# Performance work log

Measured on AMD Instinct MI355X. Metric: run time of the kernel, lower is better.

Reference implementation:

```python
import jax, jax.numpy as jnp
import numpy as np

B, T, C, H, W = 2, 8, 256, 24, 24
NH = 8
HC = C // NH          # 32 head channels
KT, KHW = 3, 9        # offset conv kernel
ST, SHW = 2, 8        # offset conv stride
EPS = 1e-5


def _p(key, shape):
    return jax.random.normal(key, shape, dtype=jnp.float32) * 0.05


def setup_inputs() -> dict:
    ks = jax.random.split(jax.random.key(0), 16)
    return {
        "x": jax.random.normal(ks[0], (B, T, C, H, W), dtype=jnp.float32),
        "w_in": _p(ks[1], (C, C)), "b_in": _p(ks[2], (C,)),
        "w_q": _p(ks[3], (C, C)), "b_q": _p(ks[4], (C,)),
        "w_off_dw": _p(ks[5], (HC, 1, KT, KHW, KHW)), "b_off_dw": _p(ks[6], (HC,)),
        "ln_g": jnp.ones((HC,), jnp.float32), "ln_b": jnp.zeros((HC,), jnp.float32),
        "w_off_proj": _p(ks[7], (3, HC)),
        "w_k": _p(ks[8], (C, C)), "b_k": _p(ks[9], (C,)),
        "w_v": _p(ks[10], (C, C)), "b_v": _p(ks[11], (C,)),
        "rpe_w1": _p(ks[12], (32, 3)), "rpe_b1": _p(ks[13], (32,)),
        "rpe_w2": _p(ks[14], (1, 32)),
    }


def _conv1x1(x, w, b):
    # x: (B,C,T,H,W), w: (Co,Ci) -> pointwise Conv3d
    return jnp.einsum('bcthw,oc->bothw', x, w) + b[None, :, None, None, None]


def _trilinear(img, gx, gy, gz):
    # torch F.grid_sample(mode='bilinear', align_corners=True) for 5D input.
    # img: (G,Ch,T,H,W); gx->W axis, gy->H axis, gz->T axis, coords in [-1,1], shape (G,S)
    G, Ch, Td, Hd, Wd = img.shape
    ix = (gx + 1.0) * 0.5 * (Wd - 1)
    iy = (gy + 1.0) * 0.5 * (Hd - 1)
    iz = (gz + 1.0) * 0.5 * (Td - 1)
    x0 = jnp.floor(ix); y0 = jnp.floor(iy); z0 = jnp.floor(iz)
    fx = ix - x0; fy = iy - y0; fz = iz - z0
    x0i = jnp.clip(x0.astype(jnp.int32), 0, Wd - 1); x1i = jnp.clip(x0i + 1, 0, Wd - 1)
    y0i = jnp.clip(y0.astype(jnp.int32), 0, Hd - 1); y1i = jnp.clip(y0i + 1, 0, Hd - 1)
    z0i = jnp.clip(z0.astype(jnp.int32), 0, Td - 1); z1i = jnp.clip(z0i + 1, 0, Td - 1)
    bidx = jnp.arange(G)[:, None]

    def g(zi, yi, xi):
        return img[bidx, :, zi, yi, xi]  # (G,S,Ch)

    wz0, wz1 = (1.0 - fz)[..., None], fz[..., None]
    wy0, wy1 = (1.0 - fy)[..., None], fy[..., None]
    wx0, wx1 = (1.0 - fx)[..., None], fx[..., None]
    return (g(z0i, y0i, x0i) * wz0 * wy0 * wx0 + g(z0i, y0i, x1i) * wz0 * wy0 * wx1 +
            g(z0i, y1i, x0i) * wz0 * wy1 * wx0 + g(z0i, y1i, x1i) * wz0 * wy1 * wx1 +
            g(z1i, y0i, x0i) * wz1 * wy0 * wx0 + g(z1i, y0i, x1i) * wz1 * wy0 * wx1 +
            g(z1i, y1i, x0i) * wz1 * wy1 * wx0 + g(z1i, y1i, x1i) * wz1 * wy1 * wx1)


def reference(x, w_in, b_in, w_q, b_q, w_off_dw, b_off_dw, ln_g, ln_b, w_off_proj,
              w_k, b_k, w_v, b_v, rpe_w1, rpe_b1, rpe_w2):
    scale = HC ** (-0.5)
    xc = _conv1x1(jnp.transpose(x, (0, 2, 1, 3, 4)), w_in, b_in)       # (B,C,T,H,W)
    q = _conv1x1(xc, w_q, b_q)
    q_off = q.reshape(B * NH, HC, T, H, W)
    # depthwise offset conv: kernel (3,9,9), stride (2,8,8), pad (1,4,4)
    off = jax.lax.conv_general_dilated(
        q_off, w_off_dw, (ST, SHW, SHW),
        ((KT // 2, KT // 2), (KHW // 2, KHW // 2), (KHW // 2, KHW // 2)),
        dimension_numbers=('NCDHW', 'OIDHW', 'NCDHW'), feature_group_count=HC)
    off = off + b_off_dw[None, :, None, None, None]
    Tk, Hk, Wk = off.shape[2], off.shape[3], off.shape[4]
    o = jnp.transpose(off, (0, 2, 3, 4, 1))                             # (G,Tk,Hk,Wk,HC)
    mu = o.mean(-1, keepdims=True)
    var = ((o - mu) ** 2).mean(-1, keepdims=True)
    o = (o - mu) / jnp.sqrt(var + EPS) * ln_g + ln_b
    o = jax.nn.gelu(o, approximate=False)
    offset = jnp.einsum('bthwc,pc->bthwp', o, w_off_proj)               # (G,Tk,Hk,Wk,3)
    # reference points (linspace(0.5, K-0.5, K) normalized by (K-1))
    rt = ((jnp.arange(Tk, dtype=jnp.float32) + 0.5) / (Tk - 1.0)) * 2.0 - 1.0
    ry = ((jnp.arange(Hk, dtype=jnp.float32) + 0.5) / (Hk - 1.0)) * 2.0 - 1.0
    rx = ((jnp.arange(Wk, dtype=jnp.float32) + 0.5) / (Wk - 1.0)) * 2.0 - 1.0
    ref = jnp.stack(jnp.meshgrid(rt, ry, rx, indexing='ij'), axis=-1)   # (Tk,Hk,Wk,3)
    pos = jnp.clip(offset + ref, -1.0, 1.0)                             # offset_range_factor < 0 path
    G = B * NH
    n = Tk * Hk * Wk
    m = T * H * W
    posf = pos.reshape(G, n, 3)                                         # (t, y, x)
    # torch passes grid = pos[..., (0,2,1)] -> grid (x_w, y_h, z_t) = (pos_t, pos_x, pos_y)
    xs = _trilinear(xc.reshape(G, HC, T, H, W), posf[..., 0], posf[..., 2], posf[..., 1])  # (G,n,HC)
    x_sampled = jnp.transpose(xs, (0, 2, 1)).reshape(B, C, Tk, Hk, Wk)
    k = _conv1x1(x_sampled, w_k, b_k).reshape(G, HC, n)
    v = _conv1x1(x_sampled, w_v, b_v).reshape(G, HC, n)
    qf = q.reshape(G, HC, m)
    attn = jnp.einsum('bcm,bcn->bmn', qf, k) * scale                    # (G,m,n)
    # log-CPB bias (source normalizes y by W-1 and x by H-1; faithful)
    qt = (jnp.arange(T, dtype=jnp.float32) / (T - 1.0)) * 2.0 - 1.0
    qy = (jnp.arange(H, dtype=jnp.float32) / (W - 1.0)) * 2.0 - 1.0
    qx = (jnp.arange(W, dtype=jnp.float32) / (H - 1.0)) * 2.0 - 1.0
    qg = jnp.stack(jnp.meshgrid(qt, qy, qx, indexing='ij'), axis=-1).reshape(m, 3)
    disp = (qg[None, :, None, :] - posf[:, None, :, :]) * 4.0           # (G,m,n,3)
    disp = jnp.sign(disp) * jnp.log2(jnp.abs(disp) + 1.0) / 3.0         # log2(8) = 3
    hbias = jax.nn.relu(jnp.einsum('gmnp,hp->gmnh', disp, rpe_w1) + rpe_b1)
    attn = attn + jnp.einsum('gmnh,oh->gmno', hbias, rpe_w2)[..., 0]
    attn = jax.nn.softmax(attn, axis=2)
    out = jnp.einsum('bmn,bcn->bcm', attn, v).reshape(B, C, T, H, W)
    return jnp.transpose(out, (0, 2, 1, 3, 4))                          # (B,T,C,H,W)
```

## Files before the change

kernel.cpp:

```cpp
#include <hip/hip_runtime.h>
#include <hip/hip_bf16.h>

typedef unsigned short ushortT;
typedef __attribute__((ext_vector_type(8))) short bf16x8;
typedef __attribute__((ext_vector_type(4))) float f32x4;
typedef __fp16 half2v __attribute__((ext_vector_type(2)));

#define WS_XC   0
#define WS_QB   2359296
#define WS_POS  3538944
#define WS_K    3540736
#define WS_V    3559168
#define WS_WC   3577600
#define WS_B512 3675904
#define WS_BIAS 3676416

__device__ __forceinline__ float bf2f(ushortT u) {
  union { unsigned int i; float f; } c; c.i = ((unsigned int)u) << 16; return c.f;
}
__device__ __forceinline__ ushortT f2bf(float f) {
  union { float f; unsigned int i; } c; c.f = f;
  unsigned int lsb = (c.i >> 16) & 1;
  return (ushortT)((c.i + 0x7fff + lsb) >> 16);
}
__device__ __forceinline__ float ldg_f(const void* p, int i, int bf) {
  return bf ? bf2f(((const ushortT*)p)[i]) : ((const float*)p)[i];
}
__device__ __forceinline__ int detect_bf(const void* x) {
  const ushortT* u = (const ushortT*)x;
  int wild = 0;
#pragma unroll
  for (int i = 0; i < 32; i++) {
    int e = (u[i] >> 7) & 0xFF;
    wild += (e != 0 && (e < 90 || e > 160)) ? 1 : 0;
  }
  return wild <= 4;
}
__device__ __forceinline__ float logmap(float d) {
  return copysignf(__log2f(fabsf(d) + 1.f) * (1.f / 3.f), d);
}

__global__ __launch_bounds__(256) void k_wc(const void* x, const void* w_in, const void* b_in,
                                            const void* w_q, const void* b_q,
                                            float* wc, float* bias512) {
  int o = blockIdx.x, tid = threadIdx.x;
  int bf = detect_bf(x);
  __shared__ float wq_s[256];
  __shared__ float red[256];
  wq_s[tid] = ldg_f(w_q, o * 256 + tid, bf);
  __syncthreads();
  float s = 0.f;
#pragma unroll 8
  for (int j = 0; j < 256; j++) s += wq_s[j] * ldg_f(w_in, j * 256 + tid, bf);
  wc[o * 256 + tid] = s;
  red[tid] = wq_s[tid] * ldg_f(b_in, tid, bf);
  __syncthreads();
  for (int m = 128; m; m >>= 1) {
    if (tid < m) red[tid] += red[tid + m];
    __syncthreads();
  }
  if (tid == 0) bias512[256 + o] = red[0] + ldg_f(b_q, o, bf);
  if (o == 0) bias512[tid] = ldg_f(b_in, tid, bf);
}

__global__ __launch_bounds__(256) void k_gemm_mfma(const void* x, const void* w_in, const float* wc,
                                                   const float* bias512, float* xc, ushortT* qb) {
  const int bf = detect_bf(x);
  __shared__ ushortT Ah[2][64 * 40], Al[2][64 * 40];
  __shared__ ushortT Bh[2][64 * 40], Bl[2][64 * 40];
  int tid = threadIdx.x;
  int bid = blockIdx.x;
  int colT = bid / 144, rowT = bid % 144;
  int col0 = colT * 64;
  int row0 = rowT * 64;
  int bt = row0 / 576;
  int hw0 = row0 % 576;
  const int isW = (col0 < 256);
  const ushortT* xB = (const ushortT*)x;
  const float*   xF = (const float*)x;
  const ushortT* wB = (const ushortT*)w_in;
  const float*   wF = (const float*)w_in;
  int ar = tid & 63, aoct = tid >> 6;
  int bn = tid >> 2, bko = tid & 3;
  int w = tid >> 6, l = tid & 63;
  int wr = w >> 1, wcq = w & 1;
  int lr = l & 15, lk = l >> 4;
  f32x4 acc[2][2] = {};

  float va[8], vb[8];
  auto loadA = [&](int kt) {
    int kbase = (bt * 256 + kt * 32 + aoct * 8) * 576 + hw0 + ar;
#pragma unroll
    for (int j = 0; j < 8; j++)
      va[j] = bf ? bf2f(xB[kbase + j * 576]) : xF[kbase + j * 576];
  };
  auto loadB = [&](int kt) {
    if (isW) {
      if (bf) {
        const ushortT* pp = wB + (col0 + bn) * 256 + kt * 32 + bko * 8;
#pragma unroll
        for (int j = 0; j < 8; j++) vb[j] = bf2f(pp[j]);
      } else {
        const float* pp = wF + (col0 + bn) * 256 + kt * 32 + bko * 8;
        float4 f0 = *(const float4*)pp;
        float4 f1 = *(const float4*)(pp + 4);
        vb[0] = f0.x; vb[1] = f0.y; vb[2] = f0.z; vb[3] = f0.w;
        vb[4] = f1.x; vb[5] = f1.y; vb[6] = f1.z; vb[7] = f1.w;
      }
    } else {
      const float* pp = wc + (col0 - 256 + bn) * 256 + kt * 32 + bko * 8;
      float4 f0 = *(const float4*)pp;
      float4 f1 = *(const float4*)(pp + 4);
      vb[0] = f0.x; vb[1] = f0.y; vb[2] = f0.z; vb[3] = f0.w;
      vb[4] = f1.x; vb[5] = f1.y; vb[6] = f1.z; vb[7] = f1.w;
    }
  };
  auto writeAB = [&](int buf) {
    unsigned ua[8], ra[8];
#pragma unroll
    for (int j = 0; j < 8; j++) {
      ua[j] = __float_as_uint(va[j]);
      ra[j] = __float_as_uint(va[j] - __uint_as_float(ua[j] & 0xffff0000u));
    }
    int4 ph, pl;
    ph.x = (int)((ua[0] >> 16) | (ua[1] & 0xffff0000u));
    ph.y = (int)((ua[2] >> 16) | (ua[3] & 0xffff0000u));
    ph.z = (int)((ua[4] >> 16) | (ua[5] & 0xffff0000u));
    ph.w = (int)((ua[6] >> 16) | (ua[7] & 0xffff0000u));
    pl.x = (int)((ra[0] >> 16) | (ra[1] & 0xffff0000u));
    pl.y = (int)((ra[2] >> 16) | (ra[3] & 0xffff0000u));
    pl.z = (int)((ra[4] >> 16) | (ra[5] & 0xffff0000u));
    pl.w = (int)((ra[6] >> 16) | (ra[7] & 0xffff0000u));
    *(int4*)&Ah[buf][ar * 40 + aoct * 8] = ph;
    *(int4*)&Al[buf][ar * 40 + aoct * 8] = pl;
#pragma unroll
    for (int j = 0; j < 8; j++) {
      ua[j] = __float_as_uint(vb[j]);
      ra[j] = __float_as_uint(vb[j] - __uint_as_float(ua[j] & 0xffff0000u));
    }
    ph.x = (int)((ua[0] >> 16) | (ua[1] & 0xffff0000u));
    ph.y = (int)((ua[2] >> 16) | (ua[3] & 0xffff0000u));
    ph.z = (int)((ua[4] >> 16) | (ua[5] & 0xffff0000u));
    ph.w = (int)((ua[6] >> 16) | (ua[7] & 0xffff0000u));
    pl.x = (int)((ra[0] >> 16) | (ra[1] & 0xffff0000u));
    pl.y = (int)((ra[2] >> 16) | (ra[3] & 0xffff0000u));
    pl.z = (int)((ra[4] >> 16) | (ra[5] & 0xffff0000u));
    pl.w = (int)((ra[6] >> 16) | (ra[7] & 0xffff0000u));
    *(int4*)&Bh[buf][bn * 40 + bko * 8] = ph;
    *(int4*)&Bl[buf][bn * 40 + bko * 8] = pl;
  };

  loadA(0); loadB(0);
  writeAB(0);
  __syncthreads();
  for (int kt = 0; kt < 8; kt++) {
    int cur = kt & 1;
    if (kt < 7) { loadA(kt + 1); loadB(kt + 1); }
    bf16x8 a0h = *(const bf16x8*)&Ah[cur][(wr * 32 + 0 * 16 + lr) * 40 + lk * 8];
    bf16x8 a1h = *(const bf16x8*)&Ah[cur][(wr * 32 + 1 * 16 + lr) * 40 + lk * 8];
    bf16x8 a0l = *(const bf16x8*)&Al[cur][(wr * 32 + 0 * 16 + lr) * 40 + lk * 8];
    bf16x8 a1l = *(const bf16x8*)&Al[cur][(wr * 32 + 1 * 16 + lr) * 40 + lk * 8];
    bf16x8 b0h = *(const bf16x8*)&Bh[cur][(wcq * 32 + 0 * 16 + lr) * 40 + lk * 8];
    bf16x8 b1h = *(const bf16x8*)&Bh[cur][(wcq * 32 + 1 * 16 + lr) * 40 + lk * 8];
    bf16x8 b0l = *(const bf16x8*)&Bl[cur][(wcq * 32 + 0 * 16 + lr) * 40 + lk * 8];
    bf16x8 b1l = *(const bf16x8*)&Bl[cur][(wcq * 32 + 1 * 16 + lr) * 40 + lk * 8];
    acc[0][0] = __builtin_amdgcn_mfma_f32_16x16x32_bf16(a0h, b0h, acc[0][0], 0, 0, 0);
    acc[0][0] = __builtin_amdgcn_mfma_f32_16x16x32_bf16(a0h, b0l, acc[0][0], 0, 0, 0);
    acc[0][0] = __builtin_amdgcn_mfma_f32_16x16x32_bf16(a0l, b0h, acc[0][0], 0, 0, 0);
    acc[0][1] = __builtin_amdgcn_mfma_f32_16x16x32_bf16(a0h, b1h, acc[0][1], 0, 0, 0);
    acc[0][1] = __builtin_amdgcn_mfma_f32_16x16x32_bf16(a0h, b1l, acc[0][1], 0, 0, 0);
    acc[0][1] = __builtin_amdgcn_mfma_f32_16x16x32_bf16(a0l, b1h, acc[0][1], 0, 0, 0);
    acc[1][0] = __builtin_amdgcn_mfma_f32_16x16x32_bf16(a1h, b0h, acc[1][0], 0, 0, 0);
    acc[1][0] = __builtin_amdgcn_mfma_f32_16x16x32_bf16(a1h, b0l, acc[1][0], 0, 0, 0);
    acc[1][0] = __builtin_amdgcn_mfma_f32_16x16x32_bf16(a1l, b0h, acc[1][0], 0, 0, 0);
    acc[1][1] = __builtin_amdgcn_mfma_f32_16x16x32_bf16(a1h, b1h, acc[1][1], 0, 0, 0);
    acc[1][1] = __builtin_amdgcn_mfma_f32_16x16x32_bf16(a1h, b1l, acc[1][1], 0, 0, 0);
    acc[1][1] = __builtin_amdgcn_mfma_f32_16x16x32_bf16(a1l, b1h, acc[1][1], 0, 0, 0);
    if (kt < 7) writeAB(cur ^ 1);
    __syncthreads();
  }
#pragma unroll
  for (int m = 0; m < 2; m++) {
#pragma unroll
    for (int n = 0; n < 2; n++) {
#pragma unroll
      for (int i = 0; i < 4; i++) {
        int row = row0 + wr * 32 + m * 16 + lk * 4 + i;
        int col = col0 + wcq * 32 + n * 16 + lr;
        float v = acc[m][n][i] + bias512[col];
        if (isW) xc[row * 256 + col] = v;
        else     qb[row * 256 + (col - 256)] = f2bf(v);
      }
    }
  }
}

__global__ __launch_bounds__(256) void k_offsets(const void* x, const ushortT* qb, const void* w_dw,
                                                 const void* b_dw, const void* ln_g, const void* ln_b,
                                                 const void* w_proj, const void* rpe_w1,
                                                 const void* rpe_b1, const void* rpe_w2,
                                                 float* pos, float* biastab) {
  __shared__ float wdw[243 * 33];
  __shared__ float part[8][33];
  __shared__ float ptile[3];
  __shared__ float dts[56];
  int bid = blockIdx.x;
  int g = bid / 36, nn = bid % 36;
  int b = g >> 3, nh = g & 7;
  int tk = nn / 9, hk = (nn / 3) % 3, wk = nn % 3;
  int tid = threadIdx.x;
  int ch = tid & 31, grp = tid >> 5;
  int bf = detect_bf(x);
  for (int i = tid; i < 7776; i += 256) {
    int c = i / 243, tap = i % 243;
    wdw[tap * 33 + c] = ldg_f(w_dw, i, bf);
  }
  __syncthreads();
  float sum = 0.f;
  for (int tap = grp; tap < 243; tap += 8) {
    int dt = tap / 81, rem = tap % 81, dh = rem / 9, dw = rem % 9;
    int t = tk * 2 - 1 + dt, h = hk * 8 - 4 + dh, w = wk * 8 - 4 + dw;
    if (t < 0 || t >= 8 || h < 0 || h >= 24 || w < 0 || w >= 24) continue;
    float qv = bf2f(qb[((b * 8 + t) * 576 + h * 24 + w) * 256 + nh * 32 + ch]);
    sum += qv * wdw[tap * 33 + ch];
  }
  part[grp][ch] = sum;
  __syncthreads();
  if (tid < 32) {
    float v = ldg_f(b_dw, ch, bf);
#pragma unroll
    for (int j = 0; j < 8; j++) v += part[j][ch];
    float s1 = v;
    for (int m = 16; m; m >>= 1) s1 += __shfl_xor(s1, m);
    float mu = s1 * (1.f / 32.f);
    float d = v - mu;
    float s2 = d * d;
    for (int m = 16; m; m >>= 1) s2 += __shfl_xor(s2, m);
    float o = d * rsqrtf(s2 * (1.f / 32.f) + 1e-5f) * ldg_f(ln_g, ch, bf) + ldg_f(ln_b, ch, bf);
    o = 0.5f * o * (1.f + erff(o * 0.70710678118654752f));
    float res[3];
#pragma unroll
    for (int p = 0; p < 3; p++) {
      float t3 = o * ldg_f(w_proj, p * 32 + ch, bf);
      for (int m = 16; m; m >>= 1) t3 += __shfl_xor(t3, m);
      res[p] = t3;
    }
    if (ch == 0) {
      float ref0 = ((tk + 0.5f) / 3.f) * 2.f - 1.f;
      float ref1 = ((hk + 0.5f) / 2.f) * 2.f - 1.f;
      float ref2 = ((wk + 0.5f) / 2.f) * 2.f - 1.f;
      float p0 = fminf(1.f, fmaxf(-1.f, res[0] + ref0));
      float p1 = fminf(1.f, fmaxf(-1.f, res[1] + ref1));
      float p2 = fminf(1.f, fmaxf(-1.f, res[2] + ref2));
      pos[bid * 3 + 0] = p0;
      pos[bid * 3 + 1] = p1;
      pos[bid * 3 + 2] = p2;
      ptile[0] = p0; ptile[1] = p1; ptile[2] = p2;
    }
  }
  __syncthreads();
  if (tid < 56) {
    float dv;
    if (tid < 8)       dv = ((float)tid        * (2.f / 7.f)  - 1.f - ptile[0]) * 4.f;
    else if (tid < 32) dv = ((float)(tid - 8)  * (2.f / 23.f) - 1.f - ptile[1]) * 4.f;
    else               dv = ((float)(tid - 32) * (2.f / 23.f) - 1.f - ptile[2]) * 4.f;
    dts[tid] = logmap(dv);
  }
  __syncthreads();
  half2v wxp[16], wyp[16], wzp[16], wbp[16], w2p[16];
#pragma unroll
  for (int j = 0; j < 16; j++) {
    wxp[j] = __builtin_amdgcn_cvt_pkrtz(ldg_f(rpe_w1, (2*j)*3+0, bf), ldg_f(rpe_w1, (2*j+1)*3+0, bf));
    wyp[j] = __builtin_amdgcn_cvt_pkrtz(ldg_f(rpe_w1, (2*j)*3+1, bf), ldg_f(rpe_w1, (2*j+1)*3+1, bf));
    wzp[j] = __builtin_amdgcn_cvt_pkrtz(ldg_f(rpe_w1, (2*j)*3+2, bf), ldg_f(rpe_w1, (2*j+1)*3+2, bf));
    wbp[j] = __builtin_amdgcn_cvt_pkrtz(ldg_f(rpe_b1, 2*j, bf), ldg_f(rpe_b1, 2*j+1, bf));
    w2p[j] = __builtin_amdgcn_cvt_pkrtz(ldg_f(rpe_w2, 2*j, bf), ldg_f(rpe_w2, 2*j+1, bf));
  }
  half2v zero = __builtin_amdgcn_cvt_pkrtz(0.f, 0.f);
  float* brow = biastab + bid * 4608;
  for (int mm = tid; mm < 4608; mm += 256) {
    int t = mm / 576, hw = mm % 576, hh = hw / 24, ww = hw % 24;
    float d0 = dts[t], d1 = dts[8 + hh], d2 = dts[32 + ww];
    half2v d0h = __builtin_amdgcn_cvt_pkrtz(d0, d0);
    half2v d1h = __builtin_amdgcn_cvt_pkrtz(d1, d1);
    half2v d2h = __builtin_amdgcn_cvt_pkrtz(d2, d2);
    float s = 0.f;
#pragma unroll
    for (int j = 0; j < 16; j++) {
      half2v hb = d0h * wxp[j] + (d1h * wyp[j] + (d2h * wzp[j] + wbp[j]));
      half2v r;
      asm("v_pk_max_f16 %0, %1, %2" : "=v"(r) : "v"(hb), "v"(zero));
      asm("v_dot2_f32_f16 %0, %1, %2, %0" : "+v"(s) : "v"(r), "v"(w2p[j]));
    }
    brow[mm] = s;
  }
}

__global__ __launch_bounds__(256) void k_svkv(const void* x, const float* xc_rm, const float* pos,
                                              const void* w_k, const void* b_k,
                                              const void* w_v, const void* b_v,
                                              float* k_rm, float* v_rm) {
  int bx = blockIdx.x;
  int row = bx >> 2, quad = bx & 3;
  int sel = quad >> 1, colhalf = quad & 1;
  int b = row / 36, nn = row % 36;
  int tid = threadIdx.x;
  int bf = detect_bf(x);
  __shared__ float a[256];
  {
    int nh = tid >> 5;
    int g = b * 8 + nh;
    float p0 = pos[(g * 36 + nn) * 3 + 0];
    float p1 = pos[(g * 36 + nn) * 3 + 1];
    float p2 = pos[(g * 36 + nn) * 3 + 2];
    float ix = (p0 + 1.f) * 0.5f * 23.f;
    float iy = (p2 + 1.f) * 0.5f * 23.f;
    float iz = (p1 + 1.f) * 0.5f * 7.f;
    float x0f = floorf(ix), y0f = floorf(iy), z0f = floorf(iz);
    float fx = ix - x0f, fy = iy - y0f, fz = iz - z0f;
    int x0 = min(max((int)x0f, 0), 23), x1 = min(x0 + 1, 23);
    int y0 = min(max((int)y0f, 0), 23), y1 = min(y0 + 1, 23);
    int z0 = min(max((int)z0f, 0), 7),  z1 = min(z0 + 1, 7);
#define AT(z, y, x) xc_rm[(((b * 8 + (z)) * 576 + (y) * 24 + (x)) * 256 + tid)]
    a[tid] =
      AT(z0, y0, x0) * (1.f - fz) * (1.f - fy) * (1.f - fx) + AT(z0, y0, x1) * (1.f - fz) * (1.f - fy) * fx +
      AT(z0, y1, x0) * (1.f - fz) * fy * (1.f - fx)         + AT(z0, y1, x1) * (1.f - fz) * fy * fx +
      AT(z1, y0, x0) * fz * (1.f - fy) * (1.f - fx)         + AT(z1, y0, x1) * fz * (1.f - fy) * fx +
      AT(z1, y1, x0) * fz * fy * (1.f - fx)                 + AT(z1, y1, x1) * fz * fy * fx;
#undef AT
  }
  __syncthreads();
  const void* w = sel ? w_v : w_k;
  const void* bb = sel ? b_v : b_k;
  int col = colhalf * 128 + (tid >> 1);
  int half = tid & 1;
  int c0 = half * 128;
  float s = 0.f;
  if (bf) {
    const ushortT* wp = (const ushortT*)w + col * 256 + c0;
#pragma unroll 4
    for (int c = 0; c < 128; c += 8) {
      ushort4 k0 = *(const ushort4*)(wp + c), k1 = *(const ushort4*)(wp + c + 4);
      s += a[c0+c+0]*bf2f(k0.x) + a[c0+c+1]*bf2f(k0.y) + a[c0+c+2]*bf2f(k0.z) + a[c0+c+3]*bf2f(k0.w)
         + a[c0+c+4]*bf2f(k1.x) + a[c0+c+5]*bf2f(k1.y) + a[c0+c+6]*bf2f(k1.z) + a[c0+c+7]*bf2f(k1.w);
    }
  } else {
    const float* wp = (const float*)w + col * 256 + c0;
#pragma unroll 8
    for (int c = 0; c < 128; c += 4) {
      float4 k4 = *(const float4*)(wp + c);
      s += a[c0+c]*k4.x + a[c0+c+1]*k4.y + a[c0+c+2]*k4.z + a[c0+c+3]*k4.w;
    }
  }
  s += __shfl_xor(s, 1);
  if (half == 0) {
    float* outp = sel ? v_rm : k_rm;
    outp[row * 256 + col] = s + ldg_f(bb, col, bf);
  }
}

__global__ __launch_bounds__(256) void k_attn(const void* x, const ushortT* qb,
                                              const float* k_rm, const float* v_rm,
                                              const float* biastab, void* outp) {
  __shared__ ushortT ksb[36][32];
  __shared__ ushortT vsb[36][32];
  int g = blockIdx.y, b = g >> 3, nh = g & 7;
  int tid = threadIdx.x;
  int bf = detect_bf(x);
  for (int e = tid; e < 36 * 32; e += 256) {
    int nn = e >> 5, ch = e & 31;
    ksb[nn][ch] = f2bf(k_rm[(b * 36 + nn) * 256 + nh * 32 + ch]);
    vsb[nn][ch] = f2bf(v_rm[(b * 36 + nn) * 256 + nh * 32 + ch]);
  }
  __syncthreads();

  int sub = tid & 7, chb = sub * 4;
  int mm = blockIdx.x * 32 + (tid >> 3);
  int t = mm / 576, hw = mm % 576;
  float qreg[4];
  {
    ushort4 u = *(const ushort4*)&qb[(b * 4608 + mm) * 256 + nh * 32 + chb];
    qreg[0] = bf2f(u.x); qreg[1] = bf2f(u.y); qreg[2] = bf2f(u.z); qreg[3] = bf2f(u.w);
  }
  const float scale = 0.17677669529663687f;
  const float* brow = biastab + g * 36 * 4608 + mm;
  float p[36];
#pragma unroll
  for (int nn = 0; nn < 36; nn++) {
    ushort4 k4 = *(const ushort4*)&ksb[nn][chb];
    float s = qreg[0] * bf2f(k4.x) + qreg[1] * bf2f(k4.y)
            + qreg[2] * bf2f(k4.z) + qreg[3] * bf2f(k4.w);
    p[nn] = s * scale;
  }
#pragma unroll
  for (int nn = 0; nn < 36; nn++) {
    p[nn] += __shfl_xor(p[nn], 1);
    p[nn] += __shfl_xor(p[nn], 2);
    p[nn] += __shfl_xor(p[nn], 4);
    p[nn] += brow[nn * 4608];
  }
  float mx = -1e30f;
#pragma unroll
  for (int nn = 0; nn < 36; nn++) mx = fmaxf(mx, p[nn]);
  float se = 0.f;
#pragma unroll
  for (int nn = 0; nn < 36; nn++) {
    float e = __expf(p[nn] - mx);
    p[nn] = e;
    se += e;
  }
  float inv = 1.f / se;
  float acc[4] = {};
#pragma unroll
  for (int nn = 0; nn < 36; nn++) {
    float pr = p[nn] * inv;
    ushort4 v4 = *(const ushort4*)&vsb[nn][chb];
    acc[0] += pr * bf2f(v4.x); acc[1] += pr * bf2f(v4.y);
    acc[2] += pr * bf2f(v4.z); acc[3] += pr * bf2f(v4.w);
  }
  int obase = ((b * 8 + t) * 256 + nh * 32 + chb) * 576 + hw;
  if (bf) {
    __hip_bfloat16* o = (__hip_bfloat16*)outp;
#pragma unroll
    for (int j = 0; j < 4; j++) o[obase + j * 576] = __float2bfloat16(acc[j]);
  } else {
    float* o = (float*)outp;
#pragma unroll
    for (int j = 0; j < 4; j++) o[obase + j * 576] = acc[j];
  }
}

extern "C" void kernel_launch(void* const* d_in, const int* in_sizes, int n_in,
                              void* d_out, int out_size, void* d_ws, size_t ws_size,
                              hipStream_t stream) {
  const void* x        = d_in[0];
  const void* w_in     = d_in[1];
  const void* b_in     = d_in[2];
  const void* w_q      = d_in[3];
  const void* b_q      = d_in[4];
  const void* w_off_dw = d_in[5];
  const void* b_off_dw = d_in[6];
  const void* ln_g     = d_in[7];
  const void* ln_b     = d_in[8];
  const void* w_off_pj = d_in[9];
  const void* w_k      = d_in[10];
  const void* b_k      = d_in[11];
  const void* w_v      = d_in[12];
  const void* b_v      = d_in[13];
  const void* rpe_w1   = d_in[14];
  const void* rpe_b1   = d_in[15];
  const void* rpe_w2   = d_in[16];

  float* ws     = (float*)d_ws;
  float* xc     = ws + WS_XC;
  ushortT* qb   = (ushortT*)(ws + WS_QB);
  float* pos    = ws + WS_POS;
  float* krm    = ws + WS_K;
  float* vrm    = ws + WS_V;
  float* wcf    = ws + WS_WC;
  float* b512   = ws + WS_B512;
  float* biastab = ws + WS_BIAS;

  k_wc<<<256, 256, 0, stream>>>(x, w_in, b_in, w_q, b_q, wcf, b512);
  k_gemm_mfma<<<1152, 256, 0, stream>>>(x, w_in, wcf, b512, xc, qb);
  k_offsets<<<576, 256, 0, stream>>>(x, qb, w_off_dw, b_off_dw, ln_g, ln_b, w_off_pj,
                                     rpe_w1, rpe_b1, rpe_w2, pos, biastab);
  k_svkv<<<288, 256, 0, stream>>>(x, xc, pos, w_k, b_k, w_v, b_v, krm, vrm);
  k_attn<<<dim3(144, 16), 256, 0, stream>>>(x, qb, krm, vrm, biastab, d_out);
}
```

Before: 124.1 us.

## Split RPE bias table computation into separate high-parallelism kernel

The log-CPB bias table generation moves out of k_offsets into a new k_biastab kernel launched over 8x576 blocks, one per time slice per offset tile. k_offsets now only writes the 56 log-mapped displacement values per tile to a workspace table. The new kernel also hoists the time-axis term (d0*w_x + b1) out of the inner loop. This spreads the bias work across many more blocks, at the cost of an extra kernel launch and a small intermediate buffer.

```diff
diff --git a/kernel.cpp b/kernel.cpp
--- a/kernel.cpp
+++ b/kernel.cpp
@@ -13,7 +13,8 @@
 #define WS_V    3559168
 #define WS_WC   3577600
 #define WS_B512 3675904
-#define WS_BIAS 3676416
+#define WS_DTAB 3676416
+#define WS_BIAS 3709184
 
 __device__ __forceinline__ float bf2f(ushortT u) {
   union { unsigned int i; float f; } c; c.i = ((unsigned int)u) << 16; return c.f;
@@ -197,13 +198,10 @@
 
 __global__ __launch_bounds__(256) void k_offsets(const void* x, const ushortT* qb, const void* w_dw,
                                                  const void* b_dw, const void* ln_g, const void* ln_b,
-                                                 const void* w_proj, const void* rpe_w1,
-                                                 const void* rpe_b1, const void* rpe_w2,
-                                                 float* pos, float* biastab) {
+                                                 const void* w_proj, float* pos, float* dtab) {
   __shared__ float wdw[243 * 33];
   __shared__ float part[8][33];
   __shared__ float ptile[3];
-  __shared__ float dts[56];
   int bid = blockIdx.x;
   int g = bid / 36, nn = bid % 36;
   int b = g >> 3, nh = g & 7;
@@ -264,35 +262,49 @@
     if (tid < 8)       dv = ((float)tid        * (2.f / 7.f)  - 1.f - ptile[0]) * 4.f;
     else if (tid < 32) dv = ((float)(tid - 8)  * (2.f / 23.f) - 1.f - ptile[1]) * 4.f;
     else               dv = ((float)(tid - 32) * (2.f / 23.f) - 1.f - ptile[2]) * 4.f;
-    dts[tid] = logmap(dv);
-  }
-  __syncthreads();
-  half2v wxp[16], wyp[16], wzp[16], wbp[16], w2p[16];
-#pragma unroll
-  for (int j = 0; j < 16; j++) {
-    wxp[j] = __builtin_amdgcn_cvt_pkrtz(ldg_f(rpe_w1, (2*j)*3+0, bf), ldg_f(rpe_w1, (2*j+1)*3+0, bf));
-    wyp[j] = __builtin_amdgcn_cvt_pkrtz(ldg_f(rpe_w1, (2*j)*3+1, bf), ldg_f(rpe_w1, (2*j+1)*3+1, bf));
-    wzp[j] = __builtin_amdgcn_cvt_pkrtz(ldg_f(rpe_w1, (2*j)*3+2, bf), ldg_f(rpe_w1, (2*j+1)*3+2, bf));
-    wbp[j] = __builtin_amdgcn_cvt_pkrtz(ldg_f(rpe_b1, 2*j, bf), ldg_f(rpe_b1, 2*j+1, bf));
-    w2p[j] = __builtin_amdgcn_cvt_pkrtz(ldg_f(rpe_w2, 2*j, bf), ldg_f(rpe_w2, 2*j+1, bf));
+    dtab[bid * 56 + tid] = logmap(dv);
+  }
+}
+
+__global__ __launch_bounds__(256) void k_biastab(const void* x, const void* rpe_w1,
+                                                 const void* rpe_b1, const void* rpe_w2,
+                                                 const float* dtab, float* biastab) {
+  int t = blockIdx.x, bid = blockIdx.y;
+  int tid = threadIdx.x;
+  int bf = detect_bf(x);
+  __shared__ float dts[56];
+  if (tid < 56) dts[tid] = dtab[bid * 56 + tid];
+  __syncthreads();
+  half2v wyp[16], wzp[16], w2p[16], a0[16];
+  {
+    float d0 = dts[t];
+    half2v d0h = __builtin_amdgcn_cvt_pkrtz(d0, d0);
+#pragma unroll
+    for (int j = 0; j < 16; j++) {
+      half2v wxp = __builtin_amdgcn_cvt_pkrtz(ldg_f(rpe_w1, (2*j)*3+0, bf), ldg_f(rpe_w1, (2*j+1)*3+0, bf));
+      half2v wbp = __builtin_amdgcn_cvt_pkrtz(ldg_f(rpe_b1, 2*j, bf), ldg_f(rpe_b1, 2*j+1, bf));
+      wyp[j] = __builtin_amdgcn_cvt_pkrtz(ldg_f(rpe_w1, (2*j)*3+1, bf), ldg_f(rpe_w1, (2*j+1)*3+1, bf));
+      wzp[j] = __builtin_amdgcn_cvt_pkrtz(ldg_f(rpe_w1, (2*j)*3+2, bf), ldg_f(rpe_w1, (2*j+1)*3+2, bf));
+      w2p[j] = __builtin_amdgcn_cvt_pkrtz(ldg_f(rpe_w2, 2*j, bf), ldg_f(rpe_w2, 2*j+1, bf));
+      a0[j] = d0h * wxp + wbp;
+    }
   }
   half2v zero = __builtin_amdgcn_cvt_pkrtz(0.f, 0.f);
-  float* brow = biastab + bid * 4608;
-  for (int mm = tid; mm < 4608; mm += 256) {
-    int t = mm / 576, hw = mm % 576, hh = hw / 24, ww = hw % 24;
-    float d0 = dts[t], d1 = dts[8 + hh], d2 = dts[32 + ww];
-    half2v d0h = __builtin_amdgcn_cvt_pkrtz(d0, d0);
+  float* brow = biastab + bid * 4608 + t * 576;
+  for (int hw = tid; hw < 576; hw += 256) {
+    int hh = hw / 24, ww = hw % 24;
+    float d1 = dts[8 + hh], d2 = dts[32 + ww];
     half2v d1h = __builtin_amdgcn_cvt_pkrtz(d1, d1);
     half2v d2h = __builtin_amdgcn_cvt_pkrtz(d2, d2);
     float s = 0.f;
 #pragma unroll
     for (int j = 0; j < 16; j++) {
-      half2v hb = d0h * wxp[j] + (d1h * wyp[j] + (d2h * wzp[j] + wbp[j]));
+      half2v hb = d1h * wyp[j] + (d2h * wzp[j] + a0[j]);
       half2v r;
       asm("v_pk_max_f16 %0, %1, %2" : "=v"(r) : "v"(hb), "v"(zero));
       asm("v_dot2_f32_f16 %0, %1, %2, %0" : "+v"(s) : "v"(r), "v"(w2p[j]));
     }
-    brow[mm] = s;
+    brow[hw] = s;
   }
 }
 
@@ -451,20 +463,21 @@
   const void* rpe_b1   = d_in[15];
   const void* rpe_w2   = d_in[16];
 
-  float* ws     = (float*)d_ws;
-  float* xc     = ws + WS_XC;
-  ushortT* qb   = (ushortT*)(ws + WS_QB);
-  float* pos    = ws + WS_POS;
-  float* krm    = ws + WS_K;
-  float* vrm    = ws + WS_V;
-  float* wcf    = ws + WS_WC;
-  float* b512   = ws + WS_B512;
+  float* ws      = (float*)d_ws;
+  float* xc      = ws + WS_XC;
+  ushortT* qb    = (ushortT*)(ws + WS_QB);
+  float* pos     = ws + WS_POS;
+  float* krm     = ws + WS_K;
+  float* vrm     = ws + WS_V;
+  float* wcf     = ws + WS_WC;
+  float* b512    = ws + WS_B512;
+  float* dtab    = ws + WS_DTAB;
   float* biastab = ws + WS_BIAS;
 
   k_wc<<<256, 256, 0, stream>>>(x, w_in, b_in, w_q, b_q, wcf, b512);
   k_gemm_mfma<<<1152, 256, 0, stream>>>(x, w_in, wcf, b512, xc, qb);
-  k_offsets<<<576, 256, 0, stream>>>(x, qb, w_off_dw, b_off_dw, ln_g, ln_b, w_off_pj,
-                                     rpe_w1, rpe_b1, rpe_w2, pos, biastab);
+  k_offsets<<<576, 256, 0, stream>>>(x, qb, w_off_dw, b_off_dw, ln_g, ln_b, w_off_pj, pos, dtab);
+  k_biastab<<<dim3(8, 576), 256, 0, stream>>>(x, rpe_w1, rpe_b1, rpe_w2, dtab, biastab);
   k_svkv<<<288, 256, 0, stream>>>(x, xc, pos, w_k, b_k, w_v, b_v, krm, vrm);
   k_attn<<<dim3(144, 16), 256, 0, stream>>>(x, qb, krm, vrm, biastab, d_out);
 }
```

Result: slower. 160.1 us (+29.0%).
